# Performance work log

Hardware: AMD Instinct MI355X
Metric: run time of the kernel (lower is better)

## Reference

```python
import jax, jax.numpy as jnp
import numpy as np

B, S, H = 4, 2048, 1024

def setup_inputs() -> dict:
    key = jax.random.key(0)
    k = jax.random.split(key, 5)
    scale = 1.0 / np.sqrt(H)
    return {
        "hidden": jax.random.normal(k[0], (B, S, H), dtype=jnp.float32),
        "mask": jnp.zeros((B, 1, S, S), dtype=jnp.float32),
        "R": jax.random.normal(k[1], (S, S), dtype=jnp.float32),
        "G_w": jax.random.normal(k[2], (H, H), dtype=jnp.float32) * scale,
        "G_b": jnp.zeros((H,), dtype=jnp.float32),
        "F_w": jax.random.normal(k[3], (H, H), dtype=jnp.float32) * scale,
        "F_b": jnp.zeros((H,), dtype=jnp.float32),
    }

def reference(hidden, mask, R, G_w, G_b, F_w, F_b):
    # scores: [B, S, S] = learned random bias + additive attention mask
    scores = R + mask[:, 0]
    probs = jax.nn.softmax(scores, axis=-1)  # dropout is identity in eval mode
    values = jnp.einsum('bsh,oh->bso', hidden, G_w) + G_b  # G_linear
    out = jnp.einsum('bqk,bkh->bqh', probs, values)
    out = jnp.einsum('bsh,oh->bso', out, F_w) + F_b  # final_linear
    return out
```

## Files before the change

### kernel.cpp

```cpp
#include <hip/hip_runtime.h>
#include <hip/hip_bf16.h>

typedef __bf16 bf16x8 __attribute__((ext_vector_type(8)));
typedef __bf16 bf16x4 __attribute__((ext_vector_type(4)));
typedef float  f32x4  __attribute__((ext_vector_type(4)));

#define GPTR(p) ((__attribute__((address_space(1))) void*)(p))
#define LPTR(p) ((__attribute__((address_space(3))) void*)(p))

__global__ __launch_bounds__(256) void cvt_kernel(const float* __restrict__ x,
                                                  __bf16* __restrict__ y, long n) {
    long i = ((long)blockIdx.x * 256 + threadIdx.x) * 8;
    if (i >= n) return;
    float4 a = *reinterpret_cast<const float4*>(x + i);
    float4 c = *reinterpret_cast<const float4*>(x + i + 4);
    bf16x8 o;
    o[0] = (__bf16)a.x; o[1] = (__bf16)a.y; o[2] = (__bf16)a.z; o[3] = (__bf16)a.w;
    o[4] = (__bf16)c.x; o[5] = (__bf16)c.y; o[6] = (__bf16)c.z; o[7] = (__bf16)c.w;
    *reinterpret_cast<bf16x8*>(y + i) = o;
}

__global__ __launch_bounds__(256) void transpose_cvt_kernel(const float* __restrict__ x,
                                                            __bf16* __restrict__ y, int n) {
    __shared__ float tile[64][65];
    const int bx = blockIdx.x * 64;
    const int by = blockIdx.y * 64;
    const int t = threadIdx.x;
    const int tr = t >> 4;
    const int tc = (t & 15) * 4;
#pragma unroll
    for (int i = 0; i < 4; i++) {
        float4 v = *reinterpret_cast<const float4*>(&x[(size_t)(by + tr + i * 16) * n + bx + tc]);
        tile[tr + i * 16][tc + 0] = v.x;
        tile[tr + i * 16][tc + 1] = v.y;
        tile[tr + i * 16][tc + 2] = v.z;
        tile[tr + i * 16][tc + 3] = v.w;
    }
    __syncthreads();
    const int wr = t >> 2;
    const int wc = (t & 3) * 16;
    bf16x8 o0, o1;
#pragma unroll
    for (int j = 0; j < 8; j++) o0[j] = (__bf16)tile[wc + j][wr];
#pragma unroll
    for (int j = 0; j < 8; j++) o1[j] = (__bf16)tile[wc + 8 + j][wr];
    *reinterpret_cast<bf16x8*>(&y[(size_t)(bx + wr) * n + by + wc]) = o0;
    *reinterpret_cast<bf16x8*>(&y[(size_t)(bx + wr) * n + by + wc + 8]) = o1;
}

__global__ __launch_bounds__(256) void gemv_bias_kernel(const float* __restrict__ Fw,
                                                        const float* __restrict__ Gb,
                                                        const float* __restrict__ Fb,
                                                        float* __restrict__ b2, int H) {
    const int o = blockIdx.x;
    float s = 0.f;
    for (int h = threadIdx.x; h < H; h += 256) s += Fw[(size_t)o * H + h] * Gb[h];
#pragma unroll
    for (int off = 32; off > 0; off >>= 1) s += __shfl_xor(s, off);
    __shared__ float ss[4];
    if ((threadIdx.x & 63) == 0) ss[threadIdx.x >> 6] = s;
    __syncthreads();
    if (threadIdx.x == 0) b2[o] = ss[0] + ss[1] + ss[2] + ss[3] + Fb[o];
}

__global__ __launch_bounds__(256) void softmax_kernel(const float* __restrict__ R,
                                                      const float* __restrict__ mask,
                                                      __bf16* __restrict__ P, int S) {
    const int q = blockIdx.x, b = blockIdx.y;
    const int t = threadIdx.x;
    const int lane = t & 63, wave = t >> 6;
    const float* rrow = R + (size_t)q * S;
    const float* mrow = mask + ((size_t)b * S + q) * (size_t)S;
    __bf16* prow = P + ((size_t)b * S + q) * (size_t)S;

    float v[8];
#pragma unroll
    for (int i = 0; i < 2; i++) {
        float4 r4 = *reinterpret_cast<const float4*>(rrow + t * 8 + i * 4);
        float4 m4 = *reinterpret_cast<const float4*>(mrow + t * 8 + i * 4);
        v[i * 4 + 0] = r4.x + m4.x;
        v[i * 4 + 1] = r4.y + m4.y;
        v[i * 4 + 2] = r4.z + m4.z;
        v[i * 4 + 3] = r4.w + m4.w;
    }
    float mx = v[0];
#pragma unroll
    for (int i = 1; i < 8; i++) mx = fmaxf(mx, v[i]);
#pragma unroll
    for (int off = 32; off > 0; off >>= 1) mx = fmaxf(mx, __shfl_xor(mx, off));
    __shared__ float smax[4], ssum[4];
    if (lane == 0) smax[wave] = mx;
    __syncthreads();
    mx = fmaxf(fmaxf(smax[0], smax[1]), fmaxf(smax[2], smax[3]));
    float sum = 0.f;
#pragma unroll
    for (int i = 0; i < 8; i++) { v[i] = __expf(v[i] - mx); sum += v[i]; }
#pragma unroll
    for (int off = 32; off > 0; off >>= 1) sum += __shfl_xor(sum, off);
    if (lane == 0) ssum[wave] = sum;
    __syncthreads();
    sum = ssum[0] + ssum[1] + ssum[2] + ssum[3];
    const float inv = 1.0f / sum;
    bf16x8 o;
#pragma unroll
    for (int i = 0; i < 8; i++) o[i] = (__bf16)(v[i] * inv);
    *reinterpret_cast<bf16x8*>(prow + t * 8) = o;
}

template <bool TRANSC, bool CFLOAT, bool BIAS>
__global__ __launch_bounds__(256) void gemm_nt_kernel(
    const __bf16* __restrict__ A, const __bf16* __restrict__ B,
    const float* __restrict__ bias, void* __restrict__ Cv,
    int K, int lda, int ldb, int ldc,
    long strideA, long strideB, long strideC) {
    const int t = threadIdx.x;
    const int lane = t & 63;
    const int wave = t >> 6;
    const int lane16 = lane & 15;
    const int quad = lane >> 4;
    const int wm = (wave >> 1) * 64;
    const int wn = (wave & 1) * 64;
    const int bm = blockIdx.y * 128;
    const int bn = blockIdx.x * 128;
    const int bz = blockIdx.z;

    A += (size_t)bz * strideA;
    B += (size_t)bz * strideB;

    __shared__ __bf16 As[128 * 64];
    __shared__ __bf16 Bs[128 * 64];

    const int rsub = lane >> 3;
    const int csub = lane & 7;
    const int lchunk = csub ^ rsub;
    const __bf16* ga0 = A + (size_t)(bm + wave * 32 + rsub) * lda + lchunk * 8;
    const __bf16* gb0 = B + (size_t)(bn + wave * 32 + rsub) * ldb + lchunk * 8;

    f32x4 acc[4][4];
#pragma unroll
    for (int i = 0; i < 4; i++)
#pragma unroll
        for (int j = 0; j < 4; j++) acc[i][j] = (f32x4){0.f, 0.f, 0.f, 0.f};

    for (int kt = 0; kt < K; kt += 64) {
        __syncthreads();
#pragma unroll
        for (int c = 0; c < 4; c++)
            __builtin_amdgcn_global_load_lds(GPTR(ga0 + (size_t)(c * 8) * lda + kt),
                                             LPTR(&As[(wave * 32 + c * 8) * 64]), 16, 0, 0);
#pragma unroll
        for (int c = 0; c < 4; c++)
            __builtin_amdgcn_global_load_lds(GPTR(gb0 + (size_t)(c * 8) * ldb + kt),
                                             LPTR(&Bs[(wave * 32 + c * 8) * 64]), 16, 0, 0);
        __syncthreads();
#pragma unroll
        for (int s = 0; s < 2; s++) {
            bf16x8 af[4], bfr[4];
#pragma unroll
            for (int mi = 0; mi < 4; mi++) {
                const int r = wm + mi * 16 + lane16;
                af[mi] = *reinterpret_cast<const bf16x8*>(
                    &As[r * 64 + (((s * 4 + quad) ^ (r & 7)) << 3)]);
            }
#pragma unroll
            for (int ni = 0; ni < 4; ni++) {
                const int r = wn + ni * 16 + lane16;
                bfr[ni] = *reinterpret_cast<const bf16x8*>(
                    &Bs[r * 64 + (((s * 4 + quad) ^ (r & 7)) << 3)]);
            }
#pragma unroll
            for (int mi = 0; mi < 4; mi++)
#pragma unroll
                for (int ni = 0; ni < 4; ni++)
                    acc[mi][ni] = __builtin_amdgcn_mfma_f32_16x16x32_bf16(af[mi], bfr[ni], acc[mi][ni], 0, 0, 0);
        }
    }

    __bf16* Cb = (__bf16*)Cv + (size_t)bz * strideC;
    float* Cf = (float*)Cv + (size_t)bz * strideC;
#pragma unroll
    for (int mi = 0; mi < 4; mi++) {
#pragma unroll
        for (int ni = 0; ni < 4; ni++) {
            const int cm = bm + wm + mi * 16 + quad * 4;
            const int cn = bn + wn + ni * 16 + lane16;
            const float bv = BIAS ? bias[cn] : 0.0f;
            if constexpr (TRANSC) {
                bf16x4 pk;
#pragma unroll
                for (int r = 0; r < 4; r++) pk[r] = (__bf16)(acc[mi][ni][r] + bv);
                *reinterpret_cast<bf16x4*>(Cb + (size_t)cn * ldc + cm) = pk;
            } else if constexpr (CFLOAT) {
#pragma unroll
                for (int r = 0; r < 4; r++)
                    Cf[(size_t)(cm + r) * ldc + cn] = acc[mi][ni][r] + bv;
            } else {
#pragma unroll
                for (int r = 0; r < 4; r++)
                    Cb[(size_t)(cm + r) * ldc + cn] = (__bf16)(acc[mi][ni][r] + bv);
            }
        }
    }
}

extern "C" void kernel_launch(void* const* d_in, const int* in_sizes, int n_in,
                              void* d_out, int out_size, void* d_ws, size_t ws_size,
                              hipStream_t stream) {
    const float* hidden = (const float*)d_in[0];
    const float* mask   = (const float*)d_in[1];
    const float* R      = (const float*)d_in[2];
    const float* G_w    = (const float*)d_in[3];
    const float* G_b    = (const float*)d_in[4];
    const float* F_w    = (const float*)d_in[5];
    const float* F_b    = (const float*)d_in[6];
    float* out = (float*)d_out;

    constexpr int B = 4, S = 2048, H = 1024;
    char* ws = (char*)d_ws;
    __bf16* h_bf  = (__bf16*)(ws);
    __bf16* vt    = (__bf16*)(ws + (16ll << 20));
    __bf16* probs = (__bf16*)(ws + (32ll << 20));
    __bf16* Wm    = (__bf16*)(ws + (32ll << 20));
    __bf16* f_bf  = (__bf16*)(ws + (64ll << 20));
    __bf16* gt_bf = (__bf16*)(ws + (66ll << 20));
    float*  b2    = (float*)(ws + (64ll << 20));

    cvt_kernel<<<(H * H) / 8 / 256, 256, 0, stream>>>(F_w, f_bf, (long)H * H);
    transpose_cvt_kernel<<<dim3(H / 64, H / 64), 256, 0, stream>>>(G_w, gt_bf, H);

    gemm_nt_kernel<false, false, false><<<dim3(H / 128, H / 128, 1), 256, 0, stream>>>(
        f_bf, gt_bf, nullptr, Wm, H, H, H, H, 0, 0, 0);

    gemv_bias_kernel<<<H, 256, 0, stream>>>(F_w, G_b, F_b, b2, H);

    cvt_kernel<<<(B * S * H) / 8 / 256, 256, 0, stream>>>(hidden, h_bf, (long)B * S * H);

    gemm_nt_kernel<true, false, false><<<dim3(H / 128, S / 128, B), 256, 0, stream>>>(
        h_bf, Wm, nullptr, vt, H, H, H,  S,
        (long)S * H, 0, (long)H * S);

    softmax_kernel<<<dim3(S, B), 256, 0, stream>>>(R, mask, probs, S);

    gemm_nt_kernel<false, true, true><<<dim3(H / 128, S / 128, B), 256, 0, stream>>>(
        probs, vt, b2, out, S, S, S, H,
        (long)S * S, (long)H * S, (long)S * H);
}
```

Baseline: 266.5 us.

## Switch GEMMs to 32x32x16 MFMA and use 64x64 tiles for weight fusion GEMM

Replaces the 16x16x32 bf16 MFMA tiling with 32x32x16 MFMA in the main NT GEMM, giving each wave a 2x2 grid of 32x32 accumulators and adjusting LDS fragment addressing and epilogue row mapping to match. It also adds a dedicated 64x64-tile GEMM kernel for the small HxH weight-combination product, launching four times as many blocks so more CUs are busy. The larger MFMA cuts instruction count and LDS reads per FLOP, but the epilogue writes less contiguously and register pressure shifts.

```diff
diff --git a/kernel.cpp b/kernel.cpp
--- a/kernel.cpp
+++ b/kernel.cpp
@@ -4,6 +4,7 @@
 typedef __bf16 bf16x8 __attribute__((ext_vector_type(8)));
 typedef __bf16 bf16x4 __attribute__((ext_vector_type(4)));
 typedef float  f32x4  __attribute__((ext_vector_type(4)));
+typedef float  f32x16 __attribute__((ext_vector_type(16)));
 
 #define GPTR(p) ((__attribute__((address_space(1))) void*)(p))
 #define LPTR(p) ((__attribute__((address_space(3))) void*)(p))
@@ -116,8 +117,8 @@
     const int t = threadIdx.x;
     const int lane = t & 63;
     const int wave = t >> 6;
-    const int lane16 = lane & 15;
-    const int quad = lane >> 4;
+    const int lane31 = lane & 31;
+    const int hi = lane >> 5;
     const int wm = (wave >> 1) * 64;
     const int wn = (wave & 1) * 64;
     const int bm = blockIdx.y * 128;
@@ -136,11 +137,11 @@
     const __bf16* ga0 = A + (size_t)(bm + wave * 32 + rsub) * lda + lchunk * 8;
     const __bf16* gb0 = B + (size_t)(bn + wave * 32 + rsub) * ldb + lchunk * 8;
 
-    f32x4 acc[4][4];
-#pragma unroll
-    for (int i = 0; i < 4; i++)
-#pragma unroll
-        for (int j = 0; j < 4; j++) acc[i][j] = (f32x4){0.f, 0.f, 0.f, 0.f};
+    f32x16 acc[2][2];
+#pragma unroll
+    for (int i = 0; i < 2; i++)
+#pragma unroll
+        for (int j = 0; j < 2; j++) acc[i][j] = (f32x16)(0.f);
 
     for (int kt = 0; kt < K; kt += 64) {
         __syncthreads();
@@ -154,52 +155,114 @@
                                              LPTR(&Bs[(wave * 32 + c * 8) * 64]), 16, 0, 0);
         __syncthreads();
 #pragma unroll
-        for (int s = 0; s < 2; s++) {
-            bf16x8 af[4], bfr[4];
-#pragma unroll
-            for (int mi = 0; mi < 4; mi++) {
-                const int r = wm + mi * 16 + lane16;
+        for (int s = 0; s < 4; s++) {
+            bf16x8 af[2], bfr[2];
+#pragma unroll
+            for (int mi = 0; mi < 2; mi++) {
+                const int r = wm + mi * 32 + lane31;
                 af[mi] = *reinterpret_cast<const bf16x8*>(
-                    &As[r * 64 + (((s * 4 + quad) ^ (r & 7)) << 3)]);
+                    &As[r * 64 + (((2 * s + hi) ^ (r & 7)) << 3)]);
             }
 #pragma unroll
-            for (int ni = 0; ni < 4; ni++) {
-                const int r = wn + ni * 16 + lane16;
+            for (int ni = 0; ni < 2; ni++) {
+                const int r = wn + ni * 32 + lane31;
                 bfr[ni] = *reinterpret_cast<const bf16x8*>(
-                    &Bs[r * 64 + (((s * 4 + quad) ^ (r & 7)) << 3)]);
+                    &Bs[r * 64 + (((2 * s + hi) ^ (r & 7)) << 3)]);
             }
 #pragma unroll
-            for (int mi = 0; mi < 4; mi++)
-#pragma unroll
-                for (int ni = 0; ni < 4; ni++)
-                    acc[mi][ni] = __builtin_amdgcn_mfma_f32_16x16x32_bf16(af[mi], bfr[ni], acc[mi][ni], 0, 0, 0);
+            for (int mi = 0; mi < 2; mi++)
+#pragma unroll
+                for (int ni = 0; ni < 2; ni++)
+                    acc[mi][ni] = __builtin_amdgcn_mfma_f32_32x32x16_bf16(af[mi], bfr[ni], acc[mi][ni], 0, 0, 0);
         }
     }
 
     __bf16* Cb = (__bf16*)Cv + (size_t)bz * strideC;
     float* Cf = (float*)Cv + (size_t)bz * strideC;
 #pragma unroll
-    for (int mi = 0; mi < 4; mi++) {
-#pragma unroll
-        for (int ni = 0; ni < 4; ni++) {
-            const int cm = bm + wm + mi * 16 + quad * 4;
-            const int cn = bn + wn + ni * 16 + lane16;
+    for (int mi = 0; mi < 2; mi++) {
+#pragma unroll
+        for (int ni = 0; ni < 2; ni++) {
+            const int cm = bm + wm + mi * 32;
+            const int cn = bn + wn + ni * 32 + lane31;
             const float bv = BIAS ? bias[cn] : 0.0f;
-            if constexpr (TRANSC) {
-                bf16x4 pk;
-#pragma unroll
-                for (int r = 0; r < 4; r++) pk[r] = (__bf16)(acc[mi][ni][r] + bv);
-                *reinterpret_cast<bf16x4*>(Cb + (size_t)cn * ldc + cm) = pk;
-            } else if constexpr (CFLOAT) {
-#pragma unroll
-                for (int r = 0; r < 4; r++)
-                    Cf[(size_t)(cm + r) * ldc + cn] = acc[mi][ni][r] + bv;
-            } else {
-#pragma unroll
-                for (int r = 0; r < 4; r++)
-                    Cb[(size_t)(cm + r) * ldc + cn] = (__bf16)(acc[mi][ni][r] + bv);
+#pragma unroll
+            for (int rq = 0; rq < 4; rq++) {
+                const int rbase = rq * 8 + 4 * hi;
+                if constexpr (TRANSC) {
+                    bf16x4 pk;
+#pragma unroll
+                    for (int rr = 0; rr < 4; rr++) pk[rr] = (__bf16)(acc[mi][ni][rq * 4 + rr] + bv);
+                    *reinterpret_cast<bf16x4*>(Cb + (size_t)cn * ldc + cm + rbase) = pk;
+                } else if constexpr (CFLOAT) {
+#pragma unroll
+                    for (int rr = 0; rr < 4; rr++)
+                        Cf[(size_t)(cm + rbase + rr) * ldc + cn] = acc[mi][ni][rq * 4 + rr] + bv;
+                } else {
+#pragma unroll
+                    for (int rr = 0; rr < 4; rr++)
+                        Cb[(size_t)(cm + rbase + rr) * ldc + cn] = (__bf16)(acc[mi][ni][rq * 4 + rr] + bv);
+                }
             }
         }
+    }
+}
+
+__global__ __launch_bounds__(256) void gemm_nt64_kernel(
+    const __bf16* __restrict__ A, const __bf16* __restrict__ B,
+    __bf16* __restrict__ C, int K, int lda, int ldb, int ldc) {
+    const int t = threadIdx.x;
+    const int lane = t & 63;
+    const int wave = t >> 6;
+    const int lane31 = lane & 31;
+    const int hi = lane >> 5;
+    const int wm = (wave >> 1) * 32;
+    const int wn = (wave & 1) * 32;
+    const int bm = blockIdx.y * 64;
+    const int bn = blockIdx.x * 64;
+
+    __shared__ __bf16 As[64 * 64];
+    __shared__ __bf16 Bs[64 * 64];
+
+    const int rsub = lane >> 3;
+    const int csub = lane & 7;
+    const int lchunk = csub ^ rsub;
+    const __bf16* ga0 = A + (size_t)(bm + wave * 16 + rsub) * lda + lchunk * 8;
+    const __bf16* gb0 = B + (size_t)(bn + wave * 16 + rsub) * ldb + lchunk * 8;
+
+    f32x16 acc = (f32x16)(0.f);
+
+    for (int kt = 0; kt < K; kt += 64) {
+        __syncthreads();
+#pragma unroll
+        for (int c = 0; c < 2; c++)
+            __builtin_amdgcn_global_load_lds(GPTR(ga0 + (size_t)(c * 8) * lda + kt),
+                                             LPTR(&As[(wave * 16 + c * 8) * 64]), 16, 0, 0);
+#pragma unroll
+        for (int c = 0; c < 2; c++)
+            __builtin_amdgcn_global_load_lds(GPTR(gb0 + (size_t)(c * 8) * ldb + kt),
+                                             LPTR(&Bs[(wave * 16 + c * 8) * 64]), 16, 0, 0);
+        __syncthreads();
+#pragma unroll
+        for (int s = 0; s < 4; s++) {
+            const int ra = wm + lane31;
+            const int rb = wn + lane31;
+            bf16x8 af = *reinterpret_cast<const bf16x8*>(
+                &As[ra * 64 + (((2 * s + hi) ^ (ra & 7)) << 3)]);
+            bf16x8 bfr = *reinterpret_cast<const bf16x8*>(
+                &Bs[rb * 64 + (((2 * s + hi) ^ (rb & 7)) << 3)]);
+            acc = __builtin_amdgcn_mfma_f32_32x32x16_bf16(af, bfr, acc, 0, 0, 0);
+        }
+    }
+
+    const int cm = bm + wm;
+    const int cn = bn + wn + lane31;
+#pragma unroll
+    for (int rq = 0; rq < 4; rq++) {
+        const int rbase = rq * 8 + 4 * hi;
+#pragma unroll
+        for (int rr = 0; rr < 4; rr++)
+            C[(size_t)(cm + rbase + rr) * ldc + cn] = (__bf16)acc[rq * 4 + rr];
     }
 }
 
@@ -228,8 +291,8 @@
     cvt_kernel<<<(H * H) / 8 / 256, 256, 0, stream>>>(F_w, f_bf, (long)H * H);
     transpose_cvt_kernel<<<dim3(H / 64, H / 64), 256, 0, stream>>>(G_w, gt_bf, H);
 
-    gemm_nt_kernel<false, false, false><<<dim3(H / 128, H / 128, 1), 256, 0, stream>>>(
-        f_bf, gt_bf, nullptr, Wm, H, H, H, H, 0, 0, 0);
+    gemm_nt64_kernel<<<dim3(H / 64, H / 64), 256, 0, stream>>>(
+        f_bf, gt_bf, Wm, H, H, H, H);
 
     gemv_bias_kernel<<<H, 256, 0, stream>>>(F_w, G_b, F_b, b2, H);
 
```

After: 257.1 us. 1.04x faster.
